# Performance work log

Measured on AMD Instinct MI355X. Metric: run time of the kernel, lower is better.

## Reference

```python
import jax, jax.numpy as jnp
import numpy as np

BN_EPS = 1e-5

def _hmu(x, mu, lam, v):
    """HMULayer forward, type='exp'.
    x:(b,d) mu:(n,d) lam:(n,) v:(n,k,d) -> (b,n)
    quad = diff @ (lam*I + V^T V) @ diff, expanded so the (n,d,d)
    Hessian and the (b,n,d) diff tensor are never materialized:
      lam*||diff||^2 = lam*(||x||^2 - 2 x.mu + ||mu||^2)
      sum_k (v_k . diff)^2, with v_k.diff = v_k.x - v_k.mu
    """
    d = x.shape[1]
    sq = (jnp.sum(x * x, axis=-1)[:, None]
          - 2.0 * (x @ mu.T)
          + jnp.sum(mu * mu, axis=-1)[None, :])               # (b,n)
    v_mu = jnp.sum(v * mu[:, None, :], axis=-1)               # (n,k)
    proj = jnp.einsum('bd,nkd->bnk', x, v) - v_mu[None]       # (b,n,k)
    quad = lam[None, :] * sq + jnp.sum(proj * proj, axis=-1)  # (b,n)
    return jnp.exp(-quad / d)

def _bn(y, gamma, beta):
    # BatchNorm1d in training mode: biased batch stats over axis 0
    m = jnp.mean(y, axis=0)
    var = jnp.mean((y - m) ** 2, axis=0)
    return (y - m) * jax.lax.rsqrt(var + BN_EPS) * gamma + beta

def setup_inputs() -> dict:
    key = jax.random.key(0)
    ks = jax.random.split(key, 8)
    b, d, n, k = 4096, 1024, 1024, 4
    x = jax.random.uniform(ks[0], (b, d), dtype=jnp.float32)
    # mu ~ U(0,1), lambda ~ 0.01*U(0,1) (k>0 branch), v ~ approx row-orthonormal
    mu1 = jax.random.uniform(ks[1], (n, d), dtype=jnp.float32)
    lam1 = 0.01 * jax.random.uniform(ks[2], (n,), dtype=jnp.float32)
    v1 = jax.random.normal(ks[3], (n, k, d), dtype=jnp.float32) / np.sqrt(d)
    mu2 = jax.random.uniform(ks[4], (n, n), dtype=jnp.float32)
    lam2 = 0.01 * jax.random.uniform(ks[5], (n,), dtype=jnp.float32)
    v2 = jax.random.normal(ks[6], (n, k, n), dtype=jnp.float32) / np.sqrt(n)
    g1 = jnp.ones((n,), jnp.float32); b1 = jnp.zeros((n,), jnp.float32)
    g2 = jnp.ones((n,), jnp.float32); b2 = jnp.zeros((n,), jnp.float32)
    return {"x": x, "mu1": mu1, "lam1": lam1, "v1": v1, "g1": g1, "b1": b1,
            "mu2": mu2, "lam2": lam2, "v2": v2, "g2": g2, "b2": b2}

def reference(x, mu1, lam1, v1, g1, b1, mu2, lam2, v2, g2, b2):
    h = _bn(_hmu(x, mu1, lam1, v1), g1, b1)     # (b, n)
    out = _bn(_hmu(h, mu2, lam2, v2), g2, b2)   # (b, n)
    return out + x  # identity shortcut (in_planes == planes, stride == 1)
```

## Files before the change

kernel.cpp:

```cpp
#include <hip/hip_runtime.h>
#include <cstdint>
#include <cstddef>

#define NB 4096
#define ND 1024

typedef unsigned short ushortT;
typedef short short8 __attribute__((ext_vector_type(8)));
typedef float f32x4 __attribute__((ext_vector_type(4)));

__device__ __forceinline__ ushortT f2bf(float f) {
    unsigned u = __float_as_uint(f);
    u += 0x7FFFu + ((u >> 16) & 1u);
    return (ushortT)(u >> 16);
}

__device__ __forceinline__ float block_sum_256(float v, float* red) {
    #pragma unroll
    for (int o = 32; o > 0; o >>= 1) v += __shfl_down(v, o, 64);
    int wave = threadIdx.x >> 6;
    if ((threadIdx.x & 63) == 0) red[wave] = v;
    __syncthreads();
    return red[0] + red[1] + red[2] + red[3];
}

__global__ void prep_x(const float* __restrict__ x, ushortT* __restrict__ xh,
                       float* __restrict__ xx) {
    __shared__ float red[4];
    int r = blockIdx.x;
    const float* row = x + (size_t)r * ND;
    ushortT* orow = xh + (size_t)r * ND;
    float s = 0.f;
    #pragma unroll
    for (int j = 0; j < 4; ++j) {
        int c = threadIdx.x + j * 256;
        float v = row[c];
        orow[c] = f2bf(v);
        s += v * v;
    }
    float tot = block_sum_256(s, red);
    if (threadIdx.x == 0) xx[r] = tot;
}

__global__ void prep_w(const float* __restrict__ mu, const float* __restrict__ v,
                       ushortT* __restrict__ W, float* __restrict__ mm,
                       float* __restrict__ vmu) {
    __shared__ float red[4];
    int bid = blockIdx.x;
    int t = bid >> 10;
    int n = bid & 1023;
    const float* src = (t == 0) ? (mu + (size_t)n * ND)
                                : (v + ((size_t)n * 4 + (t - 1)) * ND);
    const float* murow = mu + (size_t)n * ND;
    ushortT* dst = W + ((size_t)t * 1024 + n) * ND;
    float s = 0.f;
    #pragma unroll
    for (int j = 0; j < 4; ++j) {
        int c = threadIdx.x + j * 256;
        float val = src[c];
        dst[c] = f2bf(val);
        s += val * murow[c];
    }
    float tot = block_sum_256(s, red);
    if (threadIdx.x == 0) {
        if (t == 0) mm[n] = tot;
        else        vmu[n * 4 + (t - 1)] = tot;
    }
}

__launch_bounds__(256, 2)
__global__ void gemm_hmu(const ushortT* __restrict__ Xh, const ushortT* __restrict__ Wh,
                         const float* __restrict__ xx, const float* __restrict__ mm,
                         const float* __restrict__ vmu, const float* __restrict__ lam,
                         float* __restrict__ U) {
    __shared__ ushortT As[128 * 64];
    __shared__ ushortT Bs[5 * 64 * 64];
    const int tid = threadIdx.x;
    const int lane = tid & 63, wave = tid >> 6;
    const int n0 = (blockIdx.x & 15) * 64;
    const int m0 = (blockIdx.x >> 4) * 128;

    f32x4 acc[2][4][5];
    #pragma unroll
    for (int mf = 0; mf < 2; ++mf)
        #pragma unroll
        for (int nf = 0; nf < 4; ++nf)
            #pragma unroll
            for (int t = 0; t < 5; ++t)
                acc[mf][nf][t] = (f32x4){0.f, 0.f, 0.f, 0.f};

    for (int kt = 0; kt < 16; ++kt) {
        const int k0 = kt * 64;
        #pragma unroll
        for (int q = 0; q < 4; ++q) {
            int c = tid + 256 * q;
            int row = c >> 3, p = c & 7, s = p ^ (row & 7);
            uint4 d = *reinterpret_cast<const uint4*>(
                Xh + (size_t)(m0 + row) * ND + k0 + s * 8);
            *reinterpret_cast<uint4*>(&As[row * 64 + p * 8]) = d;
        }
        #pragma unroll
        for (int q = 0; q < 10; ++q) {
            int c = tid + 256 * q;
            int t = c >> 9, r = (c >> 3) & 63, p = c & 7, s = p ^ (r & 7);
            uint4 d = *reinterpret_cast<const uint4*>(
                Wh + ((size_t)t * 1024 + n0 + r) * ND + k0 + s * 8);
            *reinterpret_cast<uint4*>(&Bs[(t * 64 + r) * 64 + p * 8]) = d;
        }
        __syncthreads();
        #pragma unroll
        for (int i = 0; i < 2; ++i) {
            short8 av[2];
            #pragma unroll
            for (int mf = 0; mf < 2; ++mf) {
                int row = wave * 32 + mf * 16 + (lane & 15);
                int sl = (4 * i + (lane >> 4)) ^ (row & 7);
                av[mf] = *reinterpret_cast<const short8*>(&As[row * 64 + sl * 8]);
            }
            #pragma unroll
            for (int t = 0; t < 5; ++t) {
                #pragma unroll
                for (int nf = 0; nf < 4; ++nf) {
                    int r = nf * 16 + (lane & 15);
                    int sl = (4 * i + (lane >> 4)) ^ (r & 7);
                    short8 bv = *reinterpret_cast<const short8*>(&Bs[(t * 64 + r) * 64 + sl * 8]);
                    acc[0][nf][t] = __builtin_amdgcn_mfma_f32_16x16x32_bf16(av[0], bv, acc[0][nf][t], 0, 0, 0);
                    acc[1][nf][t] = __builtin_amdgcn_mfma_f32_16x16x32_bf16(av[1], bv, acc[1][nf][t], 0, 0, 0);
                }
            }
        }
        __syncthreads();
    }

    #pragma unroll
    for (int mf = 0; mf < 2; ++mf) {
        #pragma unroll
        for (int nf = 0; nf < 4; ++nf) {
            int col = n0 + nf * 16 + (lane & 15);
            float lamc = lam[col], mmc = mm[col];
            const float4 vm = *reinterpret_cast<const float4*>(vmu + col * 4);
            #pragma unroll
            for (int i = 0; i < 4; ++i) {
                int brow = m0 + wave * 32 + mf * 16 + (lane >> 4) * 4 + i;
                float s0 = acc[mf][nf][0][i];
                float p0 = acc[mf][nf][1][i] - vm.x;
                float p1 = acc[mf][nf][2][i] - vm.y;
                float p2 = acc[mf][nf][3][i] - vm.z;
                float p3 = acc[mf][nf][4][i] - vm.w;
                float q = lamc * (xx[brow] - 2.f * s0 + mmc)
                        + p0 * p0 + p1 * p1 + p2 * p2 + p3 * p3;
                U[(size_t)brow * ND + col] = expm1f(-q * (1.0f / 1024.0f));
            }
        }
    }
}

__global__ void colstats(const float* __restrict__ U, float* __restrict__ sum,
                         float* __restrict__ sumsq) {
    int col = blockIdx.x * 256 + threadIdx.x;
    int r0 = blockIdx.y * 128;
    float s = 0.f, q = 0.f;
    for (int j = 0; j < 128; ++j) {
        float v = U[(size_t)(r0 + j) * ND + col];
        s += v; q += v * v;
    }
    atomicAdd(&sum[col], s);
    atomicAdd(&sumsq[col], q);
}

__global__ void bn_finalize(const float* __restrict__ sum, const float* __restrict__ sumsq,
                            const float* __restrict__ g, const float* __restrict__ beta,
                            float* __restrict__ A, float* __restrict__ Bsh) {
    int c = blockIdx.x * 256 + threadIdx.x;
    float m = sum[c] * (1.0f / 4096.0f);
    float var = sumsq[c] * (1.0f / 4096.0f) - m * m;
    float a = rsqrtf(var + 1e-5f) * g[c];
    A[c] = a;
    Bsh[c] = beta[c] - m * a;
}

__global__ void bn_apply_h(const float* __restrict__ U, const float* __restrict__ A,
                           const float* __restrict__ Bsh, ushortT* __restrict__ hh,
                           float* __restrict__ xx2) {
    __shared__ float red[4];
    int r = blockIdx.x;
    float s = 0.f;
    #pragma unroll
    for (int j = 0; j < 4; ++j) {
        int c = threadIdx.x + j * 256;
        float h = U[(size_t)r * ND + c] * A[c] + Bsh[c];
        hh[(size_t)r * ND + c] = f2bf(h);
        s += h * h;
    }
    float tot = block_sum_256(s, red);
    if (threadIdx.x == 0) xx2[r] = tot;
}

__global__ void bn_apply_out(const float* __restrict__ U, const float* __restrict__ A,
                             const float* __restrict__ Bsh, const float* __restrict__ x,
                             float* __restrict__ out) {
    const int total = NB * ND;
    int stride = gridDim.x * blockDim.x;
    for (int i = blockIdx.x * blockDim.x + threadIdx.x; i < total; i += stride) {
        int c = i & 1023;
        out[i] = U[i] * A[c] + Bsh[c] + x[i];
    }
}

extern "C" void kernel_launch(void* const* d_in, const int* in_sizes, int n_in,
                              void* d_out, int out_size, void* d_ws, size_t ws_size,
                              hipStream_t stream) {
    const float* x    = (const float*)d_in[0];
    const float* mu1  = (const float*)d_in[1];
    const float* lam1 = (const float*)d_in[2];
    const float* v1   = (const float*)d_in[3];
    const float* g1   = (const float*)d_in[4];
    const float* b1   = (const float*)d_in[5];
    const float* mu2  = (const float*)d_in[6];
    const float* lam2 = (const float*)d_in[7];
    const float* v2   = (const float*)d_in[8];
    const float* g2   = (const float*)d_in[9];
    const float* b2   = (const float*)d_in[10];
    float* out = (float*)d_out;
    char* ws = (char*)d_ws;

    ushortT* xh = (ushortT*)(ws + 0);
    ushortT* hh = (ushortT*)(ws + (size_t)8  * 1024 * 1024);
    ushortT* W1 = (ushortT*)(ws + (size_t)16 * 1024 * 1024);
    ushortT* W2 = (ushortT*)(ws + (size_t)26 * 1024 * 1024 + 262144);
    float*   U  = (float*)  (ws + (size_t)36 * 1024 * 1024 + 524288);
    char* st = ws + (size_t)52 * 1024 * 1024 + 786432;
    float* xx1   = (float*)(st + 0);
    float* xx2   = (float*)(st + 16384);
    float* mm1   = (float*)(st + 32768);
    float* mm2   = (float*)(st + 36864);
    float* vmu1  = (float*)(st + 40960);
    float* vmu2  = (float*)(st + 57344);
    float* sum1  = (float*)(st + 73728);
    float* sumsq1= (float*)(st + 77824);
    float* sum2  = (float*)(st + 81920);
    float* sumsq2= (float*)(st + 86016);
    float* A1    = (float*)(st + 90112);
    float* B1s   = (float*)(st + 94208);
    float* A2    = (float*)(st + 98304);
    float* B2s   = (float*)(st + 102400);

    const size_t needed = (size_t)52 * 1024 * 1024 + 786432 + 106496;
    if (ws_size < needed) return;

    hipMemsetAsync(sum1, 0, 16384, stream);

    prep_x<<<NB, 256, 0, stream>>>(x, xh, xx1);
    prep_w<<<5120, 256, 0, stream>>>(mu1, v1, W1, mm1, vmu1);
    prep_w<<<5120, 256, 0, stream>>>(mu2, v2, W2, mm2, vmu2);

    gemm_hmu<<<512, 256, 0, stream>>>(xh, W1, xx1, mm1, vmu1, lam1, U);
    colstats<<<dim3(4, 32), 256, 0, stream>>>(U, sum1, sumsq1);
    bn_finalize<<<4, 256, 0, stream>>>(sum1, sumsq1, g1, b1, A1, B1s);
    bn_apply_h<<<NB, 256, 0, stream>>>(U, A1, B1s, hh, xx2);

    gemm_hmu<<<512, 256, 0, stream>>>(hh, W2, xx2, mm2, vmu2, lam2, U);
    colstats<<<dim3(4, 32), 256, 0, stream>>>(U, sum2, sumsq2);
    bn_finalize<<<4, 256, 0, stream>>>(sum2, sumsq2, g2, b2, A2, B2s);
    bn_apply_out<<<2048, 256, 0, stream>>>(U, A2, B2s, x, out);
}
```

Before: 241.3 us.

## Fuse prep kernels and BN stats into GEMM epilogue, use direct global-to-LDS loads

Merges the three prep kernels and the stats memset into one launch. Folds the per-column BatchNorm sum and sum-of-squares into the GEMM epilogue with atomics, and computes the BN scale and shift inline in the apply kernels. This removes the colstats and bn_finalize kernels and an extra read of U. The GEMM wave tiling changes so each wave owns 16 columns across all 128 rows, and tiles are staged with global_load_lds instead of register round-trips. The risks are higher register pressure from 40 accumulators per wave plus 8 A fragments, and atomic contention on the column sums.

```diff
diff --git a/kernel.cpp b/kernel.cpp
--- a/kernel.cpp
+++ b/kernel.cpp
@@ -24,10 +24,9 @@
     return red[0] + red[1] + red[2] + red[3];
 }
 
-__global__ void prep_x(const float* __restrict__ x, ushortT* __restrict__ xh,
-                       float* __restrict__ xx) {
-    __shared__ float red[4];
-    int r = blockIdx.x;
+__device__ __forceinline__ void prep_x_body(const float* __restrict__ x,
+                                            ushortT* __restrict__ xh,
+                                            float* __restrict__ xx, int r, float* red) {
     const float* row = x + (size_t)r * ND;
     ushortT* orow = xh + (size_t)r * ND;
     float s = 0.f;
@@ -42,11 +41,11 @@
     if (threadIdx.x == 0) xx[r] = tot;
 }
 
-__global__ void prep_w(const float* __restrict__ mu, const float* __restrict__ v,
-                       ushortT* __restrict__ W, float* __restrict__ mm,
-                       float* __restrict__ vmu) {
-    __shared__ float red[4];
-    int bid = blockIdx.x;
+__device__ __forceinline__ void prep_w_body(const float* __restrict__ mu,
+                                            const float* __restrict__ v,
+                                            ushortT* __restrict__ W,
+                                            float* __restrict__ mm,
+                                            float* __restrict__ vmu, int bid, float* red) {
     int t = bid >> 10;
     int n = bid & 1023;
     const float* src = (t == 0) ? (mu + (size_t)n * ND)
@@ -68,11 +67,32 @@
     }
 }
 
+__global__ void prep_all(const float* __restrict__ x,
+                         const float* __restrict__ mu1, const float* __restrict__ v1,
+                         const float* __restrict__ mu2, const float* __restrict__ v2,
+                         ushortT* __restrict__ xh, ushortT* __restrict__ W1,
+                         ushortT* __restrict__ W2,
+                         float* __restrict__ xx1,
+                         float* __restrict__ mm1, float* __restrict__ vmu1,
+                         float* __restrict__ mm2, float* __restrict__ vmu2,
+                         float* __restrict__ statz) {
+    __shared__ float red[4];
+    int bid = blockIdx.x;
+    if (bid < 4096)        prep_x_body(x, xh, xx1, bid, red);
+    else if (bid < 9216)   prep_w_body(mu1, v1, W1, mm1, vmu1, bid - 4096, red);
+    else if (bid < 14336)  prep_w_body(mu2, v2, W2, mm2, vmu2, bid - 9216, red);
+    else {
+        int i = (bid - 14336) * 512 + threadIdx.x * 2;
+        *reinterpret_cast<float2*>(statz + i) = make_float2(0.f, 0.f);
+    }
+}
+
 __launch_bounds__(256, 2)
 __global__ void gemm_hmu(const ushortT* __restrict__ Xh, const ushortT* __restrict__ Wh,
                          const float* __restrict__ xx, const float* __restrict__ mm,
                          const float* __restrict__ vmu, const float* __restrict__ lam,
-                         float* __restrict__ U) {
+                         float* __restrict__ U, float* __restrict__ sum,
+                         float* __restrict__ sumsq) {
     __shared__ ushortT As[128 * 64];
     __shared__ ushortT Bs[5 * 64 * 64];
     const int tid = threadIdx.x;
@@ -80,107 +100,94 @@
     const int n0 = (blockIdx.x & 15) * 64;
     const int m0 = (blockIdx.x >> 4) * 128;
 
-    f32x4 acc[2][4][5];
-    #pragma unroll
-    for (int mf = 0; mf < 2; ++mf)
-        #pragma unroll
-        for (int nf = 0; nf < 4; ++nf)
-            #pragma unroll
-            for (int t = 0; t < 5; ++t)
-                acc[mf][nf][t] = (f32x4){0.f, 0.f, 0.f, 0.f};
+    f32x4 acc[8][5];
+    #pragma unroll
+    for (int mf = 0; mf < 8; ++mf)
+        #pragma unroll
+        for (int t = 0; t < 5; ++t)
+            acc[mf][t] = (f32x4){0.f, 0.f, 0.f, 0.f};
+
+    const int lrow8 = lane >> 3;
+    const int lp    = lane & 7;
 
     for (int kt = 0; kt < 16; ++kt) {
         const int k0 = kt * 64;
         #pragma unroll
         for (int q = 0; q < 4; ++q) {
-            int c = tid + 256 * q;
-            int row = c >> 3, p = c & 7, s = p ^ (row & 7);
-            uint4 d = *reinterpret_cast<const uint4*>(
-                Xh + (size_t)(m0 + row) * ND + k0 + s * 8);
-            *reinterpret_cast<uint4*>(&As[row * 64 + p * 8]) = d;
+            int chunk = q * 4 + wave;
+            int row = chunk * 8 + lrow8;
+            int s = lp ^ (row & 7);
+            const ushortT* src = Xh + (size_t)(m0 + row) * ND + k0 + s * 8;
+            __builtin_amdgcn_global_load_lds(
+                (const __attribute__((address_space(1))) void*)src,
+                (__attribute__((address_space(3))) void*)(As + chunk * 512), 16, 0, 0);
         }
         #pragma unroll
         for (int q = 0; q < 10; ++q) {
-            int c = tid + 256 * q;
-            int t = c >> 9, r = (c >> 3) & 63, p = c & 7, s = p ^ (r & 7);
-            uint4 d = *reinterpret_cast<const uint4*>(
-                Wh + ((size_t)t * 1024 + n0 + r) * ND + k0 + s * 8);
-            *reinterpret_cast<uint4*>(&Bs[(t * 64 + r) * 64 + p * 8]) = d;
+            int chunk = q * 4 + wave;
+            int row = chunk * 8 + lrow8;
+            int t = row >> 6, rr = row & 63;
+            int s = lp ^ (row & 7);
+            const ushortT* src = Wh + ((size_t)t * 1024 + n0 + rr) * ND + k0 + s * 8;
+            __builtin_amdgcn_global_load_lds(
+                (const __attribute__((address_space(1))) void*)src,
+                (__attribute__((address_space(3))) void*)(Bs + chunk * 512), 16, 0, 0);
         }
         __syncthreads();
         #pragma unroll
         for (int i = 0; i < 2; ++i) {
-            short8 av[2];
+            short8 av[8];
             #pragma unroll
-            for (int mf = 0; mf < 2; ++mf) {
-                int row = wave * 32 + mf * 16 + (lane & 15);
+            for (int mf = 0; mf < 8; ++mf) {
+                int row = mf * 16 + (lane & 15);
                 int sl = (4 * i + (lane >> 4)) ^ (row & 7);
                 av[mf] = *reinterpret_cast<const short8*>(&As[row * 64 + sl * 8]);
             }
             #pragma unroll
             for (int t = 0; t < 5; ++t) {
+                int r = wave * 16 + (lane & 15);
+                int sl = (4 * i + (lane >> 4)) ^ (r & 7);
+                short8 bv = *reinterpret_cast<const short8*>(&Bs[(t * 64 + r) * 64 + sl * 8]);
                 #pragma unroll
-                for (int nf = 0; nf < 4; ++nf) {
-                    int r = nf * 16 + (lane & 15);
-                    int sl = (4 * i + (lane >> 4)) ^ (r & 7);
-                    short8 bv = *reinterpret_cast<const short8*>(&Bs[(t * 64 + r) * 64 + sl * 8]);
-                    acc[0][nf][t] = __builtin_amdgcn_mfma_f32_16x16x32_bf16(av[0], bv, acc[0][nf][t], 0, 0, 0);
-                    acc[1][nf][t] = __builtin_amdgcn_mfma_f32_16x16x32_bf16(av[1], bv, acc[1][nf][t], 0, 0, 0);
-                }
+                for (int mf = 0; mf < 8; ++mf)
+                    acc[mf][t] = __builtin_amdgcn_mfma_f32_16x16x32_bf16(av[mf], bv, acc[mf][t], 0, 0, 0);
             }
         }
         __syncthreads();
     }
 
-    #pragma unroll
-    for (int mf = 0; mf < 2; ++mf) {
-        #pragma unroll
-        for (int nf = 0; nf < 4; ++nf) {
-            int col = n0 + nf * 16 + (lane & 15);
-            float lamc = lam[col], mmc = mm[col];
-            const float4 vm = *reinterpret_cast<const float4*>(vmu + col * 4);
-            #pragma unroll
-            for (int i = 0; i < 4; ++i) {
-                int brow = m0 + wave * 32 + mf * 16 + (lane >> 4) * 4 + i;
-                float s0 = acc[mf][nf][0][i];
-                float p0 = acc[mf][nf][1][i] - vm.x;
-                float p1 = acc[mf][nf][2][i] - vm.y;
-                float p2 = acc[mf][nf][3][i] - vm.z;
-                float p3 = acc[mf][nf][4][i] - vm.w;
-                float q = lamc * (xx[brow] - 2.f * s0 + mmc)
-                        + p0 * p0 + p1 * p1 + p2 * p2 + p3 * p3;
-                U[(size_t)brow * ND + col] = expm1f(-q * (1.0f / 1024.0f));
-            }
-        }
-    }
-}
-
-__global__ void colstats(const float* __restrict__ U, float* __restrict__ sum,
-                         float* __restrict__ sumsq) {
-    int col = blockIdx.x * 256 + threadIdx.x;
-    int r0 = blockIdx.y * 128;
-    float s = 0.f, q = 0.f;
-    for (int j = 0; j < 128; ++j) {
-        float v = U[(size_t)(r0 + j) * ND + col];
-        s += v; q += v * v;
-    }
-    atomicAdd(&sum[col], s);
-    atomicAdd(&sumsq[col], q);
-}
-
-__global__ void bn_finalize(const float* __restrict__ sum, const float* __restrict__ sumsq,
-                            const float* __restrict__ g, const float* __restrict__ beta,
-                            float* __restrict__ A, float* __restrict__ Bsh) {
-    int c = blockIdx.x * 256 + threadIdx.x;
-    float m = sum[c] * (1.0f / 4096.0f);
-    float var = sumsq[c] * (1.0f / 4096.0f) - m * m;
-    float a = rsqrtf(var + 1e-5f) * g[c];
-    A[c] = a;
-    Bsh[c] = beta[c] - m * a;
-}
-
-__global__ void bn_apply_h(const float* __restrict__ U, const float* __restrict__ A,
-                           const float* __restrict__ Bsh, ushortT* __restrict__ hh,
+    const int col = n0 + wave * 16 + (lane & 15);
+    const float lamc = lam[col], mmc = mm[col];
+    const float4 vm = *reinterpret_cast<const float4*>(vmu + col * 4);
+    float csum = 0.f, csq = 0.f;
+    #pragma unroll
+    for (int mf = 0; mf < 8; ++mf) {
+        #pragma unroll
+        for (int i = 0; i < 4; ++i) {
+            int brow = m0 + mf * 16 + (lane >> 4) * 4 + i;
+            float s0 = acc[mf][0][i];
+            float p0 = acc[mf][1][i] - vm.x;
+            float p1 = acc[mf][2][i] - vm.y;
+            float p2 = acc[mf][3][i] - vm.z;
+            float p3 = acc[mf][4][i] - vm.w;
+            float q = lamc * (xx[brow] - 2.f * s0 + mmc)
+                    + p0 * p0 + p1 * p1 + p2 * p2 + p3 * p3;
+            float u = expm1f(-q * (1.0f / 1024.0f));
+            U[(size_t)brow * ND + col] = u;
+            csum += u; csq += u * u;
+        }
+    }
+    csum += __shfl_xor(csum, 16); csum += __shfl_xor(csum, 32);
+    csq  += __shfl_xor(csq, 16);  csq  += __shfl_xor(csq, 32);
+    if (lane < 16) {
+        atomicAdd(&sum[col], csum);
+        atomicAdd(&sumsq[col], csq);
+    }
+}
+
+__global__ void bn_apply_h(const float* __restrict__ U, const float* __restrict__ sum,
+                           const float* __restrict__ sumsq, const float* __restrict__ g,
+                           const float* __restrict__ beta, ushortT* __restrict__ hh,
                            float* __restrict__ xx2) {
     __shared__ float red[4];
     int r = blockIdx.x;
@@ -188,7 +195,11 @@
     #pragma unroll
     for (int j = 0; j < 4; ++j) {
         int c = threadIdx.x + j * 256;
-        float h = U[(size_t)r * ND + c] * A[c] + Bsh[c];
+        float m = sum[c] * (1.0f / 4096.0f);
+        float var = sumsq[c] * (1.0f / 4096.0f) - m * m;
+        float a = rsqrtf(var + 1e-5f) * g[c];
+        float b = beta[c] - m * a;
+        float h = U[(size_t)r * ND + c] * a + b;
         hh[(size_t)r * ND + c] = f2bf(h);
         s += h * h;
     }
@@ -196,14 +207,20 @@
     if (threadIdx.x == 0) xx2[r] = tot;
 }
 
-__global__ void bn_apply_out(const float* __restrict__ U, const float* __restrict__ A,
-                             const float* __restrict__ Bsh, const float* __restrict__ x,
+__global__ void bn_apply_out(const float* __restrict__ U, const float* __restrict__ sum,
+                             const float* __restrict__ sumsq, const float* __restrict__ g,
+                             const float* __restrict__ beta, const float* __restrict__ x,
                              float* __restrict__ out) {
-    const int total = NB * ND;
-    int stride = gridDim.x * blockDim.x;
-    for (int i = blockIdx.x * blockDim.x + threadIdx.x; i < total; i += stride) {
-        int c = i & 1023;
-        out[i] = U[i] * A[c] + Bsh[c] + x[i];
+    int r = blockIdx.x;
+    #pragma unroll
+    for (int j = 0; j < 4; ++j) {
+        int c = threadIdx.x + j * 256;
+        float m = sum[c] * (1.0f / 4096.0f);
+        float var = sumsq[c] * (1.0f / 4096.0f) - m * m;
+        float a = rsqrtf(var + 1e-5f) * g[c];
+        float b = beta[c] - m * a;
+        size_t idx = (size_t)r * ND + c;
+        out[idx] = U[idx] * a + b + x[idx];
     }
 }
 
@@ -240,27 +257,16 @@
     float* sumsq1= (float*)(st + 77824);
     float* sum2  = (float*)(st + 81920);
     float* sumsq2= (float*)(st + 86016);
-    float* A1    = (float*)(st + 90112);
-    float* B1s   = (float*)(st + 94208);
-    float* A2    = (float*)(st + 98304);
-    float* B2s   = (float*)(st + 102400);
 
     const size_t needed = (size_t)52 * 1024 * 1024 + 786432 + 106496;
     if (ws_size < needed) return;
 
-    hipMemsetAsync(sum1, 0, 16384, stream);
-
-    prep_x<<<NB, 256, 0, stream>>>(x, xh, xx1);
-    prep_w<<<5120, 256, 0, stream>>>(mu1, v1, W1, mm1, vmu1);
-    prep_w<<<5120, 256, 0, stream>>>(mu2, v2, W2, mm2, vmu2);
-
-    gemm_hmu<<<512, 256, 0, stream>>>(xh, W1, xx1, mm1, vmu1, lam1, U);
-    colstats<<<dim3(4, 32), 256, 0, stream>>>(U, sum1, sumsq1);
-    bn_finalize<<<4, 256, 0, stream>>>(sum1, sumsq1, g1, b1, A1, B1s);
-    bn_apply_h<<<NB, 256, 0, stream>>>(U, A1, B1s, hh, xx2);
-
-    gemm_hmu<<<512, 256, 0, stream>>>(hh, W2, xx2, mm2, vmu2, lam2, U);
-    colstats<<<dim3(4, 32), 256, 0, stream>>>(U, sum2, sumsq2);
-    bn_finalize<<<4, 256, 0, stream>>>(sum2, sumsq2, g2, b2, A2, B2s);
-    bn_apply_out<<<2048, 256, 0, stream>>>(U, A2, B2s, x, out);
-}
+    prep_all<<<14344, 256, 0, stream>>>(x, mu1, v1, mu2, v2, xh, W1, W2,
+                                        xx1, mm1, vmu1, mm2, vmu2, sum1);
+
+    gemm_hmu<<<512, 256, 0, stream>>>(xh, W1, xx1, mm1, vmu1, lam1, U, sum1, sumsq1);
+    bn_apply_h<<<NB, 256, 0, stream>>>(U, sum1, sumsq1, g1, b1, hh, xx2);
+
+    gemm_hmu<<<512, 256, 0, stream>>>(hh, W2, xx2, mm2, vmu2, lam2, U, sum2, sumsq2);
+    bn_apply_out<<<NB, 256, 0, stream>>>(U, sum2, sumsq2, g2, b2, x, out);
+}
```

Result: faster. 207.8 us (-13.8%).
